# Kernel tuning notes

Measured on AMD Instinct MI355X. Metric: run time of the kernel, lower is better.

The kernel has to match this reference:

```python
import jax, jax.numpy as jnp
import numpy as np

NUM_HEADS = 8

def setup_inputs() -> dict:
    key = jax.random.key(0)
    ks = jax.random.split(key, 12)
    B, C, H, W = 4, 256, 64, 64
    QK = 256
    NSP = 256
    x = jax.random.normal(ks[0], (B, C, H, W), dtype=jnp.float32)
    affinity_matrix = jax.random.uniform(ks[1], (B, NSP, H * W), dtype=jnp.float32)
    norm_w = 1.0 + 0.02 * jax.random.normal(ks[2], (C,), dtype=jnp.float32)
    norm_b = 0.02 * jax.random.normal(ks[3], (C,), dtype=jnp.float32)
    Wq = 0.02 * jax.random.normal(ks[4], (QK, C), dtype=jnp.float32)
    Wk = 0.02 * jax.random.normal(ks[5], (QK, C), dtype=jnp.float32)
    Wv = 0.02 * jax.random.normal(ks[6], (C, C), dtype=jnp.float32)
    Wsp = 0.02 * jax.random.normal(ks[7], (QK, C), dtype=jnp.float32)
    lepe_w = 0.02 * jax.random.normal(ks[8], (C, 1, 3, 3), dtype=jnp.float32)  # depthwise OIHW
    lepe_b = 0.02 * jax.random.normal(ks[9], (C,), dtype=jnp.float32)
    return {"x": x, "affinity_matrix": affinity_matrix, "norm_w": norm_w,
            "norm_b": norm_b, "Wq": Wq, "Wk": Wk, "Wv": Wv, "Wsp": Wsp,
            "lepe_w": lepe_w, "lepe_b": lepe_b, "num_spixels": NSP}


def _layernorm2d(x, w, b, eps=1e-6):
    # LayerNorm over channel dim of NCHW input
    xp = x.transpose(0, 2, 3, 1)  # B,H,W,C
    mu = xp.mean(-1, keepdims=True)
    var = ((xp - mu) ** 2).mean(-1, keepdims=True)
    xn = (xp - mu) * jax.lax.rsqrt(var + eps) * w + b
    return xn.transpose(0, 3, 1, 2)


def _sgca(x, affinity_matrix, norm_w, norm_b, Wq, Wk, Wv, Wsp, lepe_w, lepe_b, num_spixels):
    B, C, H, W = x.shape
    HW = H * W
    h = NUM_HEADS
    qk_dim = Wq.shape[0]
    dqk = qk_dim // h
    dv = C // h
    scale = (C // h) ** -0.5

    xn = _layernorm2d(x, norm_w, norm_b)

    # superpixel aggregation: b (hw) c
    x_flat = xn.reshape(B, C, HW).transpose(0, 2, 1)  # B,HW,C
    stoken = jnp.einsum('bmn,bnc->bmc', affinity_matrix, x_flat)
    stoken = stoken / (affinity_matrix.sum(-1, keepdims=True) + 1e-16)  # B,nsp,C

    # sp projection -> B,h,dqk,nsp
    st = jnp.einsum('bmc,qc->bmq', stoken, Wsp).transpose(0, 2, 1)
    st = st.reshape(B, h, dqk, num_spixels)

    # 1x1 conv projections
    q = jnp.einsum('oc,bchw->bohw', Wq, xn).reshape(B, h, dqk, HW)
    k = jnp.einsum('oc,bchw->bohw', Wk, xn).reshape(B, h, dqk, HW)
    vx = jnp.einsum('oc,bchw->bohw', Wv, xn)  # B,C,H,W
    v = vx.reshape(B, h, dv, HW)

    # LePE: depthwise 3x3 conv on v(x)
    lepe = jax.lax.conv_general_dilated(
        vx, lepe_w, window_strides=(1, 1), padding=((1, 1), (1, 1)),
        feature_group_count=C, dimension_numbers=('NCHW', 'OIHW', 'NCHW'))
    lepe = lepe + lepe_b[None, :, None, None]
    # faithful to original: [B,C,HW] -> permute -> [B,HW,C] -> reshape B,C,H,W
    lepe = lepe.reshape(B, C, HW).transpose(0, 2, 1).reshape(B, C, H, W)

    # stage 1: k^T @ stoken, softmax over HW axis
    s_attn = jnp.einsum('bhdn,bhdm->bhnm', k, st) * scale  # B,h,HW,nsp
    s_attn = jax.nn.softmax(s_attn, axis=-2)
    s_out = jnp.einsum('bhdn,bhnm->bhdm', v, s_attn)  # B,h,dv,nsp

    # stage 2: stoken^T @ q, softmax over nsp axis
    x_attn = jnp.einsum('bhdm,bhdn->bhmn', st, q) * scale  # B,h,nsp,HW
    x_attn = jax.nn.softmax(x_attn, axis=-2)
    x_out = jnp.einsum('bhdm,bhmn->bhdn', s_out, x_attn).reshape(B, C, H, W)

    return x_out + lepe


def reference(x, affinity_matrix, norm_w, norm_b, Wq, Wk, Wv, Wsp, lepe_w, lepe_b, num_spixels):
    return _sgca(x, affinity_matrix, norm_w, norm_b, Wq, Wk, Wv, Wsp, lepe_w, lepe_b, num_spixels)
```

## Files before the change

kernel.cpp:

```cpp
#include <hip/hip_runtime.h>
#include <hip/hip_bf16.h>

#define BATCH 4
#define CCH   256
#define HWHW  4096
#define NSP   256
#define NHEAD 8
#define SCALE 0.17677669529663689f
#define PLANE 1048576L

typedef short bf16x8 __attribute__((ext_vector_type(8)));
typedef short bf16x4 __attribute__((ext_vector_type(4)));
typedef float f32x4  __attribute__((ext_vector_type(4)));

__device__ __forceinline__ short f2bs(float f) {
    __hip_bfloat16 h = __float2bfloat16(f);
    return *(short*)&h;
}
__device__ __forceinline__ bf16x8 cvt8(float4 a, float4 b) {
    bf16x8 p;
    p[0] = f2bs(a.x); p[1] = f2bs(a.y); p[2] = f2bs(a.z); p[3] = f2bs(a.w);
    p[4] = f2bs(b.x); p[5] = f2bs(b.y); p[6] = f2bs(b.z); p[7] = f2bs(b.w);
    return p;
}
__device__ __forceinline__ void gll16(const __hip_bfloat16* g, __hip_bfloat16* l) {
    __builtin_amdgcn_global_load_lds(
        (const __attribute__((address_space(1))) unsigned int*)(const void*)g,
        (__attribute__((address_space(3))) unsigned int*)(void*)l,
        16, 0, 0);
}

__global__ __launch_bounds__(512)
void ln_fused_kernel(const float* __restrict__ x, const float* __restrict__ w,
                     const float* __restrict__ bb,
                     const float* __restrict__ Wq, const float* __restrict__ Wk,
                     const float* __restrict__ Wv, const float* __restrict__ Wsp,
                     __hip_bfloat16* __restrict__ xn_cn,
                     __hip_bfloat16* __restrict__ xn_nc,
                     __hip_bfloat16* __restrict__ wbf)
{
    __shared__ float ps[32][64], pss[32][64];
    __shared__ float mus[64], rstds[64];
    __shared__ float wls[256], bls[256];
    int blk = blockIdx.x;
    int t = threadIdx.x;
    if (blk >= 256) {
        int sel = blk - 256;
        const float* src = (sel == 0) ? Wq : (sel == 1) ? Wk : (sel == 2) ? Wv : Wsp;
        __hip_bfloat16* dst = wbf + sel * 65536;
        for (int i = t * 4; i < 65536; i += 2048) {
            float4 f = *(const float4*)(src + i);
            __hip_bfloat16 p[4];
            p[0] = __float2bfloat16(f.x); p[1] = __float2bfloat16(f.y);
            p[2] = __float2bfloat16(f.z); p[3] = __float2bfloat16(f.w);
            *(int2*)(dst + i) = *(int2*)p;
        }
        return;
    }
    int b = blk >> 6;
    int n0 = (blk & 63) * 64;
    int pg = t & 15;
    int cq = t >> 4;
    if (t < 256) { wls[t] = w[t]; bls[t] = bb[t]; }

    const float* xp = x + ((long)(b * CCH + cq * 8)) * HWHW + n0 + pg * 4;
    float4 v[8];
#pragma unroll
    for (int i = 0; i < 8; ++i) v[i] = *(const float4*)(xp + (long)i * HWHW);
    float4 s = {0.f,0.f,0.f,0.f}, ss = {0.f,0.f,0.f,0.f};
#pragma unroll
    for (int i = 0; i < 8; ++i) {
        s.x += v[i].x; s.y += v[i].y; s.z += v[i].z; s.w += v[i].w;
        ss.x += v[i].x * v[i].x; ss.y += v[i].y * v[i].y;
        ss.z += v[i].z * v[i].z; ss.w += v[i].w * v[i].w;
    }
    *(float4*)&ps[cq][pg * 4]  = s;
    *(float4*)&pss[cq][pg * 4] = ss;
    __syncthreads();
    if (t < 64) {
        float S = 0.f, SS = 0.f;
#pragma unroll
        for (int q = 0; q < 32; ++q) { S += ps[q][t]; SS += pss[q][t]; }
        float mu = S * (1.f / 256.f);
        float var = SS * (1.f / 256.f) - mu * mu;
        mus[t] = mu; rstds[t] = rsqrtf(var + 1e-6f);
    }
    __syncthreads();
    float4 mu4 = *(float4*)&mus[pg * 4];
    float4 rs4 = *(float4*)&rstds[pg * 4];

    bf16x8 pk[4];
#pragma unroll
    for (int i = 0; i < 8; ++i) {
        int c = cq * 8 + i;
        float wc = wls[c], bc = bls[c];
        short h0 = f2bs((v[i].x - mu4.x) * rs4.x * wc + bc);
        short h1 = f2bs((v[i].y - mu4.y) * rs4.y * wc + bc);
        short h2 = f2bs((v[i].z - mu4.z) * rs4.z * wc + bc);
        short h3 = f2bs((v[i].w - mu4.w) * rs4.w * wc + bc);
        pk[0][i] = h0; pk[1][i] = h1; pk[2][i] = h2; pk[3][i] = h3;
        bf16x4 q; q[0] = h0; q[1] = h1; q[2] = h2; q[3] = h3;
        *(bf16x4*)(xn_cn + ((long)(b * CCH + c)) * HWHW + n0 + pg * 4) = q;
    }
#pragma unroll
    for (int j = 0; j < 4; ++j)
        *(bf16x8*)(xn_nc + ((long)b * HWHW + n0 + pg * 4 + j) * CCH + cq * 8) = pk[j];
}

__device__ __forceinline__ void gemm_k256_128(
    const __hip_bfloat16* __restrict__ A, const __hip_bfloat16* __restrict__ B,
    __hip_bfloat16* __restrict__ C, int bx, int by, int bz,
    int N, long aStrideZ, long bStrideZ, long cStrideZ,
    __hip_bfloat16* __restrict__ Asm)
{
    const int K = 256;
    const int t = threadIdx.x, lane = t & 63, w = t >> 6;
    const int l15 = lane & 15, quad = lane >> 4;
    const int Mt = by * 128, Nt = bx * 128;
    {
        const __hip_bfloat16* aBase = A + (long)bz * aStrideZ
            + (long)(Mt + l15) * K + quad * 8;
#pragma unroll
        for (int p = 0; p < 16; ++p) {
            const int rt = w * 2 + (p >> 3), s = p & 7;
            gll16(aBase + (long)(rt * 16) * K + s * 32, Asm + (rt * 8 + s) * 512);
        }
    }
    const int wm2 = w & 1, wn2 = w >> 1;
    const __hip_bfloat16* bBase = B + (long)bz * bStrideZ
        + (long)(Nt + wn2 * 64 + l15) * K + quad * 8;

    f32x4 acc[4][4];
#pragma unroll
    for (int mi = 0; mi < 4; ++mi)
#pragma unroll
        for (int nj = 0; nj < 4; ++nj) acc[mi][nj] = f32x4{0.f,0.f,0.f,0.f};

    bf16x8 bEv[4], bOd[4];
#pragma unroll
    for (int nj = 0; nj < 4; ++nj)
        bEv[nj] = *(const bf16x8*)(bBase + (long)(nj * 16) * K);
    __syncthreads();
#pragma unroll
    for (int sp = 0; sp < 4; ++sp) {
        const int s0 = 2 * sp, s1 = 2 * sp + 1;
#pragma unroll
        for (int nj = 0; nj < 4; ++nj)
            bOd[nj] = *(const bf16x8*)(bBase + (long)(nj * 16) * K + s1 * 32);
#pragma unroll
        for (int mi = 0; mi < 4; ++mi) {
            bf16x8 a = *(const bf16x8*)&Asm[((wm2 * 4 + mi) * 8 + s0) * 512 + lane * 8];
            acc[mi][0] = __builtin_amdgcn_mfma_f32_16x16x32_bf16(a, bEv[0], acc[mi][0], 0, 0, 0);
            acc[mi][1] = __builtin_amdgcn_mfma_f32_16x16x32_bf16(a, bEv[1], acc[mi][1], 0, 0, 0);
            acc[mi][2] = __builtin_amdgcn_mfma_f32_16x16x32_bf16(a, bEv[2], acc[mi][2], 0, 0, 0);
            acc[mi][3] = __builtin_amdgcn_mfma_f32_16x16x32_bf16(a, bEv[3], acc[mi][3], 0, 0, 0);
        }
        if (sp < 3) {
#pragma unroll
            for (int nj = 0; nj < 4; ++nj)
                bEv[nj] = *(const bf16x8*)(bBase + (long)(nj * 16) * K + (s0 + 2) * 32);
        }
#pragma unroll
        for (int mi = 0; mi < 4; ++mi) {
            bf16x8 a = *(const bf16x8*)&Asm[((wm2 * 4 + mi) * 8 + s1) * 512 + lane * 8];
            acc[mi][0] = __builtin_amdgcn_mfma_f32_16x16x32_bf16(a, bOd[0], acc[mi][0], 0, 0, 0);
            acc[mi][1] = __builtin_amdgcn_mfma_f32_16x16x32_bf16(a, bOd[1], acc[mi][1], 0, 0, 0);
            acc[mi][2] = __builtin_amdgcn_mfma_f32_16x16x32_bf16(a, bOd[2], acc[mi][2], 0, 0, 0);
            acc[mi][3] = __builtin_amdgcn_mfma_f32_16x16x32_bf16(a, bOd[3], acc[mi][3], 0, 0, 0);
        }
    }
#pragma unroll
    for (int mi = 0; mi < 4; ++mi)
#pragma unroll
        for (int nj = 0; nj < 4; ++nj)
#pragma unroll
            for (int r = 0; r < 4; ++r) {
                int m = Mt + wm2 * 64 + mi * 16 + quad * 4 + r;
                int n = Nt + wn2 * 64 + nj * 16 + l15;
                C[(long)bz * cStrideZ + (long)m * N + n] =
                    __float2bfloat16(acc[mi][nj][r]);
            }
}

template <int OUTK, int ASTAGE, bool ROWSUM, int NTL>
__device__ __forceinline__ void gemm_body(
    const void* __restrict__ Av, const __hip_bfloat16* __restrict__ B,
    void* __restrict__ Cptr, int bx, int by, int bz,
    int N, int K, int kChunk, int kShift,
    long aStrideZ, long bStrideZ, long cStrideZ,
    float* __restrict__ rsPart,
    __hip_bfloat16* __restrict__ Asm, __hip_bfloat16* __restrict__ Bsm,
    float* __restrict__ rsl)
{
    int z = bz;
    int b = z >> kShift;
    int ch = z & ((1 << kShift) - 1);
    int t = threadIdx.x;
    int lane = t & 63, w = t >> 6;
    int l15 = lane & 15, quad = lane >> 4;
    int Mt = by * 64, Nt = bx * 64 * NTL;

    if (ASTAGE == 2 && t < 64) {
        float s = 0.f;
#pragma unroll
        for (int pl = 0; pl < 8; ++pl) s += rsPart[((b * 8 + pl) << 8) + Mt + t];
        rsl[t] = s;
    }

    long aOff = (long)b * aStrideZ + (long)ch * kChunk
        + (long)(Mt + w * 16 + l15) * K + quad * 8;
    const float* aSrcF = (const float*)Av + aOff;
    const __hip_bfloat16* bSrc = B + (long)b * bStrideZ + (long)ch * kChunk
        + (long)(Nt + w * 16 + l15) * K + quad * 8;

    f32x4 acc[NTL][2][2];
#pragma unroll
    for (int nt = 0; nt < NTL; ++nt)
#pragma unroll
        for (int i = 0; i < 2; ++i)
#pragma unroll
            for (int j = 0; j < 2; ++j) acc[nt][i][j] = f32x4{0.f,0.f,0.f,0.f};
    f32x4 rs0 = {0.f,0.f,0.f,0.f}, rs1 = rs0;
    bf16x8 onesf;
    { short o = (l15 == 0) ? (short)0x3F80 : (short)0;
      onesf = bf16x8{o, o, o, o, o, o, o, o}; }
    int wm = (w & 1) * 2, wn = (w >> 1) * 2;

    float4 pf0, pf1, pf2, pf3;
    if (ASTAGE == 1) {
        pf0 = *(const float4*)(aSrcF);      pf1 = *(const float4*)(aSrcF + 4);
        pf2 = *(const float4*)(aSrcF + 32); pf3 = *(const float4*)(aSrcF + 36);
    }

    const bf16x8* AsmU = (const bf16x8*)Asm;
    const bf16x8* BsmU = (const bf16x8*)Bsm;

    for (int k0 = 0; k0 < kChunk; k0 += 64) {
        if (ASTAGE == 1) {
            *(bf16x8*)&Asm[t * 8]        = cvt8(pf0, pf1);
            *(bf16x8*)&Asm[2048 + t * 8] = cvt8(pf2, pf3);
        } else {
#pragma unroll
            for (int kh = 0; kh < 2; ++kh) {
                float4 s0 = {0.f,0.f,0.f,0.f}, s1 = {0.f,0.f,0.f,0.f};
#pragma unroll
                for (int pl = 0; pl < 8; ++pl) {
                    const float* p = aSrcF + (long)pl * 65536 + k0 + kh * 32;
                    float4 u0 = *(const float4*)p, u1 = *(const float4*)(p + 4);
                    s0.x += u0.x; s0.y += u0.y; s0.z += u0.z; s0.w += u0.w;
                    s1.x += u1.x; s1.y += u1.y; s1.z += u1.z; s1.w += u1.w;
                }
                *(bf16x8*)&Asm[kh * 2048 + t * 8] = cvt8(s0, s1);
            }
        }
#pragma unroll
        for (int nt = 0; nt < NTL; ++nt) {
            gll16(bSrc + (long)nt * 64 * K + k0,      Bsm + nt * 4096 + w * 512);
            gll16(bSrc + (long)nt * 64 * K + k0 + 32, Bsm + nt * 4096 + 2048 + w * 512);
        }
        __syncthreads();
        if (ASTAGE == 1 && k0 + 64 < kChunk) {
            const float* nx = aSrcF + k0 + 64;
            pf0 = *(const float4*)nx;        pf1 = *(const float4*)(nx + 4);
            pf2 = *(const float4*)(nx + 32); pf3 = *(const float4*)(nx + 36);
        }
#pragma unroll
        for (int kh = 0; kh < 2; ++kh) {
            bf16x8 a0 = AsmU[kh * 256 + wm * 64 + lane];
            bf16x8 a1 = AsmU[kh * 256 + (wm + 1) * 64 + lane];
            if (ROWSUM) {
                rs0 = __builtin_amdgcn_mfma_f32_16x16x32_bf16(a0, onesf, rs0, 0, 0, 0);
                rs1 = __builtin_amdgcn_mfma_f32_16x16x32_bf16(a1, onesf, rs1, 0, 0, 0);
            }
#pragma unroll
            for (int nt = 0; nt < NTL; ++nt) {
                bf16x8 b0 = BsmU[nt * 512 + kh * 256 + wn * 64 + lane];
                bf16x8 b1 = BsmU[nt * 512 + kh * 256 + (wn + 1) * 64 + lane];
                acc[nt][0][0] = __builtin_amdgcn_mfma_f32_16x16x32_bf16(a0, b0, acc[nt][0][0], 0, 0, 0);
                acc[nt][0][1] = __builtin_amdgcn_mfma_f32_16x16x32_bf16(a0, b1, acc[nt][0][1], 0, 0, 0);
                acc[nt][1][0] = __builtin_amdgcn_mfma_f32_16x16x32_bf16(a1, b0, acc[nt][1][0], 0, 0, 0);
                acc[nt][1][1] = __builtin_amdgcn_mfma_f32_16x16x32_bf16(a1, b1, acc[nt][1][1], 0, 0, 0);
            }
        }
        __syncthreads();
    }
    if (ROWSUM && bx == 0 && (w >> 1) == 0 && l15 == 0) {
#pragma unroll
        for (int r = 0; r < 4; ++r) {
            rsPart[(long)z * 256 + Mt + wm * 16 + quad * 4 + r]       = rs0[r];
            rsPart[(long)z * 256 + Mt + (wm + 1) * 16 + quad * 4 + r] = rs1[r];
        }
    }
#pragma unroll
    for (int nt = 0; nt < NTL; ++nt)
#pragma unroll
        for (int i = 0; i < 2; ++i)
#pragma unroll
            for (int j = 0; j < 2; ++j)
#pragma unroll
                for (int r = 0; r < 4; ++r) {
                    int m = Mt + (wm + i) * 16 + quad * 4 + r;
                    int n = Nt + nt * 64 + (wn + j) * 16 + l15;
                    float val = acc[nt][i][j][r];
                    if (ASTAGE == 2) val /= (rsl[m - Mt] + 1e-16f);
                    long off = (long)z * cStrideZ + (long)m * N + n;
                    if (OUTK == 0) ((float*)Cptr)[off] = val;
                    else ((__hip_bfloat16*)Cptr)[off] = __float2bfloat16(val);
                }
}

__global__ __launch_bounds__(256, 2)
void mega1_kernel(const float* __restrict__ aff,
                  const __hip_bfloat16* __restrict__ xn_cn,
                  const __hip_bfloat16* __restrict__ xn_nc,
                  const __hip_bfloat16* __restrict__ wbf,
                  __hip_bfloat16* __restrict__ qk_nc,
                  __hip_bfloat16* __restrict__ v_cn,
                  float* __restrict__ stoken_part,
                  float* __restrict__ rs_part)
{
    __shared__ __align__(16) char smem[65536];
    __hip_bfloat16* Asm = (__hip_bfloat16*)smem;
    __hip_bfloat16* Bsm = (__hip_bfloat16*)(smem + 8192);
    __hip_bfloat16* A128 = (__hip_bfloat16*)smem;
    int blk = blockIdx.x;
    if (blk < 128) {
        int i = blk;
        gemm_body<0, 1, true, 4>(aff, xn_cn, stoken_part,
            0, i >> 5, i & 31, 256, 4096, 512, 3,
            PLANE, PLANE, 65536L, rs_part, Asm, Bsm, nullptr);
    } else if (blk < 640) {
        int i = blk - 128;
        int bx = i >> 7, rem = i & 127;
        gemm_k256_128(xn_nc, wbf, qk_nc,
            bx, rem >> 2, rem & 3, 512, PLANE, 0L, 2 * PLANE, A128);
    } else {
        int i = blk - 640;
        int by = i >> 7, rem = i & 127;
        gemm_k256_128(wbf + 2 * 65536, xn_nc, v_cn,
            rem >> 2, by, rem & 3, 4096, 0L, PLANE, PLANE, A128);
    }
}

__global__ __launch_bounds__(256)
void stmd_kernel(const float* __restrict__ part,
                 const __hip_bfloat16* __restrict__ wsp,
                 __hip_bfloat16* __restrict__ st_md,
                 float* __restrict__ rs_part)
{
    __shared__ __hip_bfloat16 Asm[4096];
    __shared__ __hip_bfloat16 Bsm[4096];
    __shared__ float rsl[64];
    int i = blockIdx.x;
    gemm_body<1, 2, false, 1>(part, wsp, st_md,
        i & 3, (i >> 2) & 3, i >> 4, 256, 256, 256, 0,
        524288L, 0L, 65536L, rs_part, Asm, Bsm, rsl);
}

__device__ __forceinline__
void stage1_dev(char* smem, int chunk, int bh,
                const __hip_bfloat16* __restrict__ qk_nc,
                const __hip_bfloat16* __restrict__ v_cn,
                const __hip_bfloat16* __restrict__ st_md,
                __hip_bfloat16* __restrict__ opart)
{
    __hip_bfloat16* Es  = (__hip_bfloat16*)smem;
    __hip_bfloat16* sts = (__hip_bfloat16*)(smem + 36864);
    const int b = bh >> 3, h = bh & 7;
    const int t = threadIdx.x, lane = t & 63, w = t >> 6;
    const int l15 = lane & 15, quad = lane >> 4;
    const int n0 = chunk * 256;

    {
        const int4* src = (const int4*)(st_md + ((long)(b * 256 + t)) * 256 + h * 32);
        int4* dst = (int4*)&sts[t * 40];
        dst[0] = src[0]; dst[1] = src[1]; dst[2] = src[2]; dst[3] = src[3];
    }
    const __hip_bfloat16* kfp = qk_nc + ((long)b * 4096 + n0 + 16 * w + l15) * 512 + 256 + h * 32 + quad * 8;
    const __hip_bfloat16* vp0 = v_cn + ((long)(b * 256 + h * 32 + l15)) * 4096 + n0 + quad * 8;
    const __hip_bfloat16* vp1 = vp0 + 16 * 4096;
    bf16x8 kfs[4], vv[4][4];
    kfs[0]   = *(const bf16x8*)(kfp);
    vv[0][0] = *(const bf16x8*)(vp0);
    vv[0][1] = *(const bf16x8*)(vp1);
    vv[0][2] = *(const bf16x8*)(vp0 + 32);
    vv[0][3] = *(const bf16x8*)(vp1 + 32);
    __syncthreads();
    bf16x8 afrag[16];
#pragma unroll
    for (int mt = 0; mt < 16; ++mt)
        afrag[mt] = *(const bf16x8*)&sts[(mt * 16 + l15) * 40 + quad * 8];
    bf16x8 onesf;
    { short o = (l15 == 0) ? (short)0x3F80 : (short)0;
      onesf = bf16x8{o, o, o, o, o, o, o, o}; }

    f32x4 occ[4][3];
#pragma unroll
    for (int i = 0; i < 4; ++i)
#pragma unroll
        for (int j = 0; j < 3; ++j) occ[i][j] = f32x4{0.f,0.f,0.f,0.f};

#pragma unroll
    for (int sub = 0; sub < 4; ++sub) {
#pragma unroll
        for (int mt = 0; mt < 16; ++mt) {
            f32x4 s = __builtin_amdgcn_mfma_f32_16x16x32_bf16(afrag[mt], kfs[sub], f32x4{0.f,0.f,0.f,0.f}, 0, 0, 0);
#pragma unroll
            for (int r = 0; r < 4; ++r)
                Es[(mt * 16 + quad * 4 + r) * 72 + 16 * w + l15] =
                    __float2bfloat16(__expf(s[r] * SCALE));
        }
        if (sub < 3) {
            kfs[sub + 1]   = *(const bf16x8*)(kfp + (long)(sub + 1) * 64 * 512);
            vv[sub + 1][0] = *(const bf16x8*)(vp0 + (sub + 1) * 64);
            vv[sub + 1][1] = *(const bf16x8*)(vp1 + (sub + 1) * 64);
            vv[sub + 1][2] = *(const bf16x8*)(vp0 + (sub + 1) * 64 + 32);
            vv[sub + 1][3] = *(const bf16x8*)(vp1 + (sub + 1) * 64 + 32);
        }
        __syncthreads();
#pragma unroll
        for (int ks = 0; ks < 2; ++ks) {
            bf16x8 bf0 = vv[sub][2 * ks + 0];
            bf16x8 bf1 = vv[sub][2 * ks + 1];
#pragma unroll
            for (int mi = 0; mi < 4; ++mi) {
                bf16x8 af = *(const bf16x8*)&Es[(64 * w + mi * 16 + l15) * 72 + ks * 32 + quad * 8];
                occ[mi][0] = __builtin_amdgcn_mfma_f32_16x16x32_bf16(af, bf0, occ[mi][0], 0, 0, 0);
                occ[mi][1] = __builtin_amdgcn_mfma_f32_16x16x32_bf16(af, bf1, occ[mi][1], 0, 0, 0);
                occ[mi][2] = __builtin_amdgcn_mfma_f32_16x16x32_bf16(af, onesf, occ[mi][2], 0, 0, 0);
            }
        }
        __syncthreads();
    }
    __hip_bfloat16* tb = Es;
#pragma unroll
    for (int mi = 0; mi < 4; ++mi)
#pragma unroll
        for (int jt = 0; jt < 3; ++jt) {
            if (jt == 2 && l15 != 0) continue;
            int col = jt * 16 + l15;
#pragma unroll
            for (int r = 0; r < 4; ++r) {
                int m = 64 * w + mi * 16 + quad * 4 + r;
                tb[col * 264 + m] = __float2bfloat16(occ[mi][jt][r]);
            }
        }
    __syncthreads();
    int* og = (int*)(opart) + (long)(chunk * 32 + bh) * 4224;
    const int* tbi = (const int*)tb;
#pragma unroll
    for (int i = 0; i < 17; ++i) {
        int idx = t + i * 256;
        if (idx < 4224) {
            int row = idx >> 7, off = idx & 127;
            og[idx] = tbi[row * 132 + off];
        }
    }
}

__device__ __forceinline__
void lepe_dev(char* smem, int bx, int cy, int b,
              const __hip_bfloat16* __restrict__ v_cn,
              const float* __restrict__ lw, const float* __restrict__ lb,
              __hip_bfloat16* __restrict__ lepe_cn)
{
    __hip_bfloat16* in_t    = (__hip_bfloat16*)smem;
    __hip_bfloat16* tile_bf = (__hip_bfloat16*)(smem + 24576);
    float* wls = (float*)(smem + 41472);
    float* bls = (float*)(smem + 42624);
    const int c0 = cy * 32;
    const int t = threadIdx.x;
    const int n0 = bx * 256, r0 = bx * 4;

    for (int i = t; i < 288; i += 256) wls[i] = lw[c0 * 9 + i];
    if (t < 32)  bls[t] = lb[c0 + t];
#pragma unroll
    for (int i = 0; i < 6; ++i) {
        int vi = t + i * 256;
        int ch = vi / 48;
        int off = (vi % 48) * 8;
        int g = (r0 - 1) * 64 + off;
        int4 val = {0, 0, 0, 0};
        if ((unsigned)g < 4096u)
            val = *(const int4*)(v_cn + (((long)(b * CCH + c0 + ch)) << 12) + g);
        *(int4*)&in_t[ch * 384 + off] = val;
    }
    __syncthreads();

    const int lane = t & 63, w = t >> 6;
#pragma unroll
    for (int i = 0; i < 8; ++i) {
        int ch = w * 8 + i;
        float cr[6], lf[6], rf[6];
#pragma unroll
        for (int rr = 0; rr < 6; ++rr) {
            cr[rr] = (float)in_t[ch * 384 + rr * 64 + lane];
            float lv = __shfl_up(cr[rr], 1);
            float rv = __shfl_down(cr[rr], 1);
            lf[rr] = (lane == 0) ? 0.f : lv;
            rf[rr] = (lane == 63) ? 0.f : rv;
        }
        float w0 = wls[ch*9+0], w1 = wls[ch*9+1], w2 = wls[ch*9+2];
        float w3 = wls[ch*9+3], w4 = wls[ch*9+4], w5 = wls[ch*9+5];
        float w6 = wls[ch*9+6], w7 = wls[ch*9+7], w8 = wls[ch*9+8];
        float bias = bls[ch];
#pragma unroll
        for (int r = 0; r < 4; ++r) {
            float acc = bias
                + lf[r]   * w0 + cr[r]   * w1 + rf[r]   * w2
                + lf[r+1] * w3 + cr[r+1] * w4 + rf[r+1] * w5
                + lf[r+2] * w6 + cr[r+2] * w7 + rf[r+2] * w8;
            tile_bf[(r * 64 + lane) * 33 + ch] = __float2bfloat16(acc);
        }
    }
    __syncthreads();
#pragma unroll
    for (int i = 0; i < 32; ++i) {
        int idx = t + i * 256;
        int nl = idx >> 5, cj = idx & 31;
        int sp = n0 + nl;
        lepe_cn[((long)(b * CCH + (sp >> 4)) << 12) + (nl & 15) * 256 + c0 + cj] =
            tile_bf[nl * 33 + cj];
    }
}

__global__ __launch_bounds__(256)
void mega2_kernel(const __hip_bfloat16* __restrict__ qk_nc,
                  const __hip_bfloat16* __restrict__ v_cn,
                  const __hip_bfloat16* __restrict__ st_md,
                  __hip_bfloat16* __restrict__ opart,
                  const float* __restrict__ lw, const float* __restrict__ lb,
                  __hip_bfloat16* __restrict__ lepe_cn)
{
    __shared__ __align__(16) char smem[57344];
    int blk = blockIdx.x;
    if (blk < 512) {
        stage1_dev(smem, blk & 15, blk >> 4, qk_nc, v_cn, st_md, opart);
    } else {
        int j = blk - 512;
        lepe_dev(smem, j & 15, (j >> 4) & 7, j >> 7, v_cn, lw, lb, lepe_cn);
    }
}

__global__ __launch_bounds__(256)
void merge1_kernel(const __hip_bfloat16* __restrict__ opart, __hip_bfloat16* __restrict__ sout)
{
    int t = blockIdx.x * 256 + threadIdx.x;
    int m = t & 255;
    int d = (t >> 8) & 31;
    int bh = t >> 13;
    float num = 0.f, den = 0.f;
    for (int ch = 0; ch < 16; ++ch) {
        long base = (long)((ch * 32 + bh) * 33) * 256 + m;
        num += (float)opart[base + (long)d * 256];
        den += (float)opart[base + 32 * 256];
    }
    sout[(long)bh * 8192 + d * 256 + m] = __float2bfloat16(num / den);
}

__global__ __launch_bounds__(256)
void stage2_mfma(const __hip_bfloat16* __restrict__ qk_nc,
                 const __hip_bfloat16* __restrict__ st_md,
                 const __hip_bfloat16* __restrict__ sout_bf,
                 const __hip_bfloat16* __restrict__ lepe_cn,
                 float* __restrict__ out)
{
    __shared__ __hip_bfloat16 Es2[64 * 264];
    __shared__ __hip_bfloat16 sos[32 * 264];
    __shared__ float o_t[32 * 68];
    const int chunk = blockIdx.x, bh = blockIdx.y;
    const int b = bh >> 3, h = bh & 7;
    const int t = threadIdx.x, lane = t & 63, w = t >> 6;
    const int l15 = lane & 15, quad = lane >> 4;
    const int n0 = chunk * 256;

    {
        int row = t >> 3, seg = t & 7;
        const int4* src = (const int4*)(sout_bf + (long)bh * 8192 + row * 256 + seg * 32);
        int4* dst = (int4*)&sos[row * 264 + seg * 32];
        dst[0] = src[0]; dst[1] = src[1]; dst[2] = src[2]; dst[3] = src[3];
    }
    bf16x8 stfrag[4];
#pragma unroll
    for (int mt = 0; mt < 4; ++mt)
        stfrag[mt] = *(const bf16x8*)(st_md
            + ((long)(b * 256 + 64 * w + mt * 16 + l15)) * 256 + h * 32 + quad * 8);
    const __hip_bfloat16* qfp = qk_nc + ((long)b * 4096 + n0 + l15) * 512 + h * 32 + quad * 8;
    bf16x8 qq[4][4];
#pragma unroll
    for (int nt = 0; nt < 4; ++nt)
        qq[0][nt] = *(const bf16x8*)(qfp + (long)(nt * 16) * 512);
    bf16x8 onesf;
    { short o = (l15 == 0) ? (short)0x3F80 : (short)0;
      onesf = bf16x8{o, o, o, o, o, o, o, o}; }
    __syncthreads();

#pragma unroll
    for (int sub = 0; sub < 4; ++sub) {
        const int nbase = n0 + sub * 64;
#pragma unroll
        for (int nt = 0; nt < 4; ++nt) {
            bf16x8 qf = qq[sub][nt];
#pragma unroll
            for (int mt = 0; mt < 4; ++mt) {
                f32x4 s = __builtin_amdgcn_mfma_f32_16x16x32_bf16(qf, stfrag[mt], f32x4{0.f,0.f,0.f,0.f}, 0, 0, 0);
#pragma unroll
                for (int r = 0; r < 4; ++r)
                    Es2[(nt * 16 + quad * 4 + r) * 264 + 64 * w + mt * 16 + l15] =
                        __float2bfloat16(__expf(s[r] * SCALE));
            }
        }
        if (sub < 3) {
#pragma unroll
            for (int nt = 0; nt < 4; ++nt)
                qq[sub + 1][nt] = *(const bf16x8*)(qfp + (long)((sub + 1) * 64 + nt * 16) * 512);
        }
        __syncthreads();
        f32x4 o0 = {0.f,0.f,0.f,0.f}, o1 = o0, o2 = o0;
#pragma unroll
        for (int ks = 0; ks < 8; ++ks) {
            bf16x8 af = *(const bf16x8*)&Es2[(16 * w + l15) * 264 + ks * 32 + quad * 8];
            bf16x8 b0 = *(const bf16x8*)&sos[(l15) * 264 + ks * 32 + quad * 8];
            bf16x8 b1 = *(const bf16x8*)&sos[(16 + l15) * 264 + ks * 32 + quad * 8];
            o0 = __builtin_amdgcn_mfma_f32_16x16x32_bf16(af, b0, o0, 0, 0, 0);
            o1 = __builtin_amdgcn_mfma_f32_16x16x32_bf16(af, b1, o1, 0, 0, 0);
            o2 = __builtin_amdgcn_mfma_f32_16x16x32_bf16(af, onesf, o2, 0, 0, 0);
        }
        __syncthreads();
#pragma unroll
        for (int r = 0; r < 4; ++r) {
            float den = __shfl(o2[r], lane & 48);
            float inv = 1.f / den;
            o_t[(l15) * 68 + 16 * w + quad * 4 + r]      = o0[r] * inv;
            o_t[(16 + l15) * 68 + 16 * w + quad * 4 + r] = o1[r] * inv;
        }
        __syncthreads();
        {
            int row = t >> 3, coff = (t & 7) * 8;
            long gb = ((long)(b * 256 + h * 32 + row)) * 4096 + nbase + coff;
            int4 lp4 = *(const int4*)(lepe_cn + gb);
            const __hip_bfloat16* lp = (const __hip_bfloat16*)&lp4;
            const float* sp = &o_t[row * 68 + coff];
            float4 r0, r1;
            r0.x = sp[0] + (float)lp[0]; r0.y = sp[1] + (float)lp[1];
            r0.z = sp[2] + (float)lp[2]; r0.w = sp[3] + (float)lp[3];
            r1.x = sp[4] + (float)lp[4]; r1.y = sp[5] + (float)lp[5];
            r1.z = sp[6] + (float)lp[6]; r1.w = sp[7] + (float)lp[7];
            *(float4*)(out + gb)     = r0;
            *(float4*)(out + gb + 4) = r1;
        }
        __syncthreads();
    }
}

extern "C" void kernel_launch(void* const* d_in, const int* in_sizes, int n_in,
                              void* d_out, int out_size, void* d_ws, size_t ws_size,
                              hipStream_t stream)
{
    const float* x    = (const float*)d_in[0];
    const float* aff  = (const float*)d_in[1];
    const float* nw   = (const float*)d_in[2];
    const float* nb   = (const float*)d_in[3];
    const float* Wq   = (const float*)d_in[4];
    const float* Wk   = (const float*)d_in[5];
    const float* Wv   = (const float*)d_in[6];
    const float* Wsp  = (const float*)d_in[7];
    const float* lw   = (const float*)d_in[8];
    const float* lb   = (const float*)d_in[9];
    float* out = (float*)d_out;

    float* ws = (float*)d_ws;
    const long P = PLANE;
    __hip_bfloat16* qk_nc  = (__hip_bfloat16*)(ws);
    __hip_bfloat16* v_cn   = (__hip_bfloat16*)(ws + 4 * P);
    __hip_bfloat16* xn_cn  = (__hip_bfloat16*)(ws + 6 * P);
    __hip_bfloat16* xn_nc  = (__hip_bfloat16*)(ws + 8 * P);
    __hip_bfloat16* lepe_cn= (__hip_bfloat16*)(ws + 10 * P);
    float* stoken_part = ws + 14 * P;
    __hip_bfloat16* opart = (__hip_bfloat16*)(ws + 16 * P);
    float* tail        = ws + 16 * P + 2162688;
    __hip_bfloat16* wbf       = (__hip_bfloat16*)tail;
    __hip_bfloat16* st_md     = (__hip_bfloat16*)(tail + 262144);
    __hip_bfloat16* sout_bf   = (__hip_bfloat16*)(tail + 393216);
    float* rs_part = tail + 525312;

    ln_fused_kernel<<<260, 512, 0, stream>>>(x, nw, nb, Wq, Wk, Wv, Wsp,
                                             xn_cn, xn_nc, wbf);
    mega1_kernel<<<896, 256, 0, stream>>>(aff, xn_cn, xn_nc, wbf,
                                          qk_nc, v_cn, stoken_part, rs_part);
    stmd_kernel<<<64, 256, 0, stream>>>(stoken_part, wbf + 3 * 65536, st_md, rs_part);
    mega2_kernel<<<1024, 256, 0, stream>>>(qk_nc, v_cn, st_md, opart, lw, lb, lepe_cn);
    merge1_kernel<<<1024, 256, 0, stream>>>(opart, sout_bf);
    stage2_mfma<<<dim3(16, 32), 256, 0, stream>>>(qk_nc, st_md, sout_bf, lepe_cn, out);
}
```

Measured before the change: 195.8 us.

## Move LePE conv into stmd launch and shrink shared memory of attention kernels

Relocates the depthwise LePE blocks from the stage-1 attention launch into the small 64-block stoken projection launch, which otherwise leaves most CUs idle. The stage-1 kernel then allocates only 36 KB of LDS by aliasing the stoken staging buffer with the score buffer, behind an added barrier. Stage2 also aliases its output transpose buffer onto the score buffer. Both LDS cuts are meant to raise occupancy. The cost is extra synchronisation, and the aliasing needs correct barrier ordering.

After: 189.4 us. -3.3%, faster.

```diff
diff --git a/kernel.cpp b/kernel.cpp
--- a/kernel.cpp
+++ b/kernel.cpp
@@ -342,30 +342,107 @@
     }
 }
 
+__device__ __forceinline__
+void lepe_dev(char* smem, int bx, int cy, int b,
+              const __hip_bfloat16* __restrict__ v_cn,
+              const float* __restrict__ lw, const float* __restrict__ lb,
+              __hip_bfloat16* __restrict__ lepe_cn)
+{
+    __hip_bfloat16* in_t    = (__hip_bfloat16*)smem;
+    __hip_bfloat16* tile_bf = (__hip_bfloat16*)(smem + 24576);
+    float* wls = (float*)(smem + 41472);
+    float* bls = (float*)(smem + 42624);
+    const int c0 = cy * 32;
+    const int t = threadIdx.x;
+    const int n0 = bx * 256, r0 = bx * 4;
+
+    for (int i = t; i < 288; i += 256) wls[i] = lw[c0 * 9 + i];
+    if (t < 32)  bls[t] = lb[c0 + t];
+#pragma unroll
+    for (int i = 0; i < 6; ++i) {
+        int vi = t + i * 256;
+        int ch = vi / 48;
+        int off = (vi % 48) * 8;
+        int g = (r0 - 1) * 64 + off;
+        int4 val = {0, 0, 0, 0};
+        if ((unsigned)g < 4096u)
+            val = *(const int4*)(v_cn + (((long)(b * CCH + c0 + ch)) << 12) + g);
+        *(int4*)&in_t[ch * 384 + off] = val;
+    }
+    __syncthreads();
+
+    const int lane = t & 63, w = t >> 6;
+#pragma unroll
+    for (int i = 0; i < 8; ++i) {
+        int ch = w * 8 + i;
+        float cr[6], lf[6], rf[6];
+#pragma unroll
+        for (int rr = 0; rr < 6; ++rr) {
+            cr[rr] = (float)in_t[ch * 384 + rr * 64 + lane];
+            float lv = __shfl_up(cr[rr], 1);
+            float rv = __shfl_down(cr[rr], 1);
+            lf[rr] = (lane == 0) ? 0.f : lv;
+            rf[rr] = (lane == 63) ? 0.f : rv;
+        }
+        float w0 = wls[ch*9+0], w1 = wls[ch*9+1], w2 = wls[ch*9+2];
+        float w3 = wls[ch*9+3], w4 = wls[ch*9+4], w5 = wls[ch*9+5];
+        float w6 = wls[ch*9+6], w7 = wls[ch*9+7], w8 = wls[ch*9+8];
+        float bias = bls[ch];
+#pragma unroll
+        for (int r = 0; r < 4; ++r) {
+            float acc = bias
+                + lf[r]   * w0 + cr[r]   * w1 + rf[r]   * w2
+                + lf[r+1] * w3 + cr[r+1] * w4 + rf[r+1] * w5
+                + lf[r+2] * w6 + cr[r+2] * w7 + rf[r+2] * w8;
+            tile_bf[(r * 64 + lane) * 33 + ch] = __float2bfloat16(acc);
+        }
+    }
+    __syncthreads();
+#pragma unroll
+    for (int i = 0; i < 32; ++i) {
+        int idx = t + i * 256;
+        int nl = idx >> 5, cj = idx & 31;
+        int sp = n0 + nl;
+        lepe_cn[((long)(b * CCH + (sp >> 4)) << 12) + (nl & 15) * 256 + c0 + cj] =
+            tile_bf[nl * 33 + cj];
+    }
+}
+
 __global__ __launch_bounds__(256)
-void stmd_kernel(const float* __restrict__ part,
-                 const __hip_bfloat16* __restrict__ wsp,
-                 __hip_bfloat16* __restrict__ st_md,
-                 float* __restrict__ rs_part)
-{
-    __shared__ __hip_bfloat16 Asm[4096];
-    __shared__ __hip_bfloat16 Bsm[4096];
-    __shared__ float rsl[64];
-    int i = blockIdx.x;
-    gemm_body<1, 2, false, 1>(part, wsp, st_md,
-        i & 3, (i >> 2) & 3, i >> 4, 256, 256, 256, 0,
-        524288L, 0L, 65536L, rs_part, Asm, Bsm, rsl);
-}
-
-__device__ __forceinline__
-void stage1_dev(char* smem, int chunk, int bh,
-                const __hip_bfloat16* __restrict__ qk_nc,
-                const __hip_bfloat16* __restrict__ v_cn,
-                const __hip_bfloat16* __restrict__ st_md,
-                __hip_bfloat16* __restrict__ opart)
-{
+void stmd_lepe_kernel(const float* __restrict__ part,
+                      const __hip_bfloat16* __restrict__ wsp,
+                      __hip_bfloat16* __restrict__ st_md,
+                      float* __restrict__ rs_part,
+                      const __hip_bfloat16* __restrict__ v_cn,
+                      const float* __restrict__ lw, const float* __restrict__ lb,
+                      __hip_bfloat16* __restrict__ lepe_cn)
+{
+    __shared__ __align__(16) char smem[43008];
+    int blk = blockIdx.x;
+    if (blk < 64) {
+        __hip_bfloat16* Asm = (__hip_bfloat16*)smem;
+        __hip_bfloat16* Bsm = (__hip_bfloat16*)(smem + 8192);
+        float* rsl = (float*)(smem + 16384);
+        int i = blk;
+        gemm_body<1, 2, false, 1>(part, wsp, st_md,
+            i & 3, (i >> 2) & 3, i >> 4, 256, 256, 256, 0,
+            524288L, 0L, 65536L, rs_part, Asm, Bsm, rsl);
+    } else {
+        int j = blk - 64;
+        lepe_dev(smem, j & 15, (j >> 4) & 7, j >> 7, v_cn, lw, lb, lepe_cn);
+    }
+}
+
+__global__ __launch_bounds__(256)
+void mega2_kernel(const __hip_bfloat16* __restrict__ qk_nc,
+                  const __hip_bfloat16* __restrict__ v_cn,
+                  const __hip_bfloat16* __restrict__ st_md,
+                  __hip_bfloat16* __restrict__ opart)
+{
+    __shared__ __align__(16) char smem[36864];
     __hip_bfloat16* Es  = (__hip_bfloat16*)smem;
-    __hip_bfloat16* sts = (__hip_bfloat16*)(smem + 36864);
+    __hip_bfloat16* sts = (__hip_bfloat16*)smem;
+    const int chunk = blockIdx.x & 15, bh = blockIdx.x >> 4;
     const int b = bh >> 3, h = bh & 7;
     const int t = threadIdx.x, lane = t & 63, w = t >> 6;
     const int l15 = lane & 15, quad = lane >> 4;
@@ -390,6 +467,7 @@
 #pragma unroll
     for (int mt = 0; mt < 16; ++mt)
         afrag[mt] = *(const bf16x8*)&sts[(mt * 16 + l15) * 40 + quad * 8];
+    __syncthreads();
     bf16x8 onesf;
     { short o = (l15 == 0) ? (short)0x3F80 : (short)0;
       onesf = bf16x8{o, o, o, o, o, o, o, o}; }
@@ -455,90 +533,6 @@
             int row = idx >> 7, off = idx & 127;
             og[idx] = tbi[row * 132 + off];
         }
-    }
-}
-
-__device__ __forceinline__
-void lepe_dev(char* smem, int bx, int cy, int b,
-              const __hip_bfloat16* __restrict__ v_cn,
-              const float* __restrict__ lw, const float* __restrict__ lb,
-              __hip_bfloat16* __restrict__ lepe_cn)
-{
-    __hip_bfloat16* in_t    = (__hip_bfloat16*)smem;
-    __hip_bfloat16* tile_bf = (__hip_bfloat16*)(smem + 24576);
-    float* wls = (float*)(smem + 41472);
-    float* bls = (float*)(smem + 42624);
-    const int c0 = cy * 32;
-    const int t = threadIdx.x;
-    const int n0 = bx * 256, r0 = bx * 4;
-
-    for (int i = t; i < 288; i += 256) wls[i] = lw[c0 * 9 + i];
-    if (t < 32)  bls[t] = lb[c0 + t];
-#pragma unroll
-    for (int i = 0; i < 6; ++i) {
-        int vi = t + i * 256;
-        int ch = vi / 48;
-        int off = (vi % 48) * 8;
-        int g = (r0 - 1) * 64 + off;
-        int4 val = {0, 0, 0, 0};
-        if ((unsigned)g < 4096u)
-            val = *(const int4*)(v_cn + (((long)(b * CCH + c0 + ch)) << 12) + g);
-        *(int4*)&in_t[ch * 384 + off] = val;
-    }
-    __syncthreads();
-
-    const int lane = t & 63, w = t >> 6;
-#pragma unroll
-    for (int i = 0; i < 8; ++i) {
-        int ch = w * 8 + i;
-        float cr[6], lf[6], rf[6];
-#pragma unroll
-        for (int rr = 0; rr < 6; ++rr) {
-            cr[rr] = (float)in_t[ch * 384 + rr * 64 + lane];
-            float lv = __shfl_up(cr[rr], 1);
-            float rv = __shfl_down(cr[rr], 1);
-            lf[rr] = (lane == 0) ? 0.f : lv;
-            rf[rr] = (lane == 63) ? 0.f : rv;
-        }
-        float w0 = wls[ch*9+0], w1 = wls[ch*9+1], w2 = wls[ch*9+2];
-        float w3 = wls[ch*9+3], w4 = wls[ch*9+4], w5 = wls[ch*9+5];
-        float w6 = wls[ch*9+6], w7 = wls[ch*9+7], w8 = wls[ch*9+8];
-        float bias = bls[ch];
-#pragma unroll
-        for (int r = 0; r < 4; ++r) {
-            float acc = bias
-                + lf[r]   * w0 + cr[r]   * w1 + rf[r]   * w2
-                + lf[r+1] * w3 + cr[r+1] * w4 + rf[r+1] * w5
-                + lf[r+2] * w6 + cr[r+2] * w7 + rf[r+2] * w8;
-            tile_bf[(r * 64 + lane) * 33 + ch] = __float2bfloat16(acc);
-        }
-    }
-    __syncthreads();
-#pragma unroll
-    for (int i = 0; i < 32; ++i) {
-        int idx = t + i * 256;
-        int nl = idx >> 5, cj = idx & 31;
-        int sp = n0 + nl;
-        lepe_cn[((long)(b * CCH + (sp >> 4)) << 12) + (nl & 15) * 256 + c0 + cj] =
-            tile_bf[nl * 33 + cj];
-    }
-}
-
-__global__ __launch_bounds__(256)
-void mega2_kernel(const __hip_bfloat16* __restrict__ qk_nc,
-                  const __hip_bfloat16* __restrict__ v_cn,
-                  const __hip_bfloat16* __restrict__ st_md,
-                  __hip_bfloat16* __restrict__ opart,
-                  const float* __restrict__ lw, const float* __restrict__ lb,
-                  __hip_bfloat16* __restrict__ lepe_cn)
-{
-    __shared__ __align__(16) char smem[57344];
-    int blk = blockIdx.x;
-    if (blk < 512) {
-        stage1_dev(smem, blk & 15, blk >> 4, qk_nc, v_cn, st_md, opart);
-    } else {
-        int j = blk - 512;
-        lepe_dev(smem, j & 15, (j >> 4) & 7, j >> 7, v_cn, lw, lb, lepe_cn);
     }
 }
 
@@ -565,9 +559,10 @@
                  const __hip_bfloat16* __restrict__ lepe_cn,
                  float* __restrict__ out)
 {
-    __shared__ __hip_bfloat16 Es2[64 * 264];
-    __shared__ __hip_bfloat16 sos[32 * 264];
-    __shared__ float o_t[32 * 68];
+    __shared__ __align__(16) char smem[50688];
+    __hip_bfloat16* Es2 = (__hip_bfloat16*)smem;
+    __hip_bfloat16* sos = (__hip_bfloat16*)(smem + 33792);
+    float* o_t = (float*)smem;
     const int chunk = blockIdx.x, bh = blockIdx.y;
     const int b = bh >> 3, h = bh & 7;
     const int t = threadIdx.x, lane = t & 63, w = t >> 6;
@@ -688,8 +683,10 @@
                                              xn_cn, xn_nc, wbf);
     mega1_kernel<<<896, 256, 0, stream>>>(aff, xn_cn, xn_nc, wbf,
                                           qk_nc, v_cn, stoken_part, rs_part);
-    stmd_kernel<<<64, 256, 0, stream>>>(stoken_part, wbf + 3 * 65536, st_md, rs_part);
-    mega2_kernel<<<1024, 256, 0, stream>>>(qk_nc, v_cn, st_md, opart, lw, lb, lepe_cn);
+    stmd_lepe_kernel<<<576, 256, 0, stream>>>(stoken_part, wbf + 3 * 65536,
+                                              st_md, rs_part,
+                                              v_cn, lw, lb, lepe_cn);
+    mega2_kernel<<<512, 256, 0, stream>>>(qk_nc, v_cn, st_md, opart);
     merge1_kernel<<<1024, 256, 0, stream>>>(opart, sout_bf);
     stage2_mfma<<<dim3(16, 32), 256, 0, stream>>>(qk_nc, st_md, sout_bf, lepe_cn, out);
 }
```
